# Optimization experiments

Measured on AMD Instinct MI355X. Metric: run time of the kernel, lower is better.

Reference implementation:

```python
import jax, jax.numpy as jnp
import numpy as np

B, L, D_MODEL = 8, 2048, 256
D_STATE, D_CONV, EXPAND, DT_RANK = 8, 4, 2, 2
D_INNER = EXPAND * D_MODEL
CHUNK = 32  # chunkSize in _parallelScan


def setup_inputs() -> dict:
    key = jax.random.key(0)
    ks = jax.random.split(key, 8)
    def nrm(k, shape, fan_in):
        return jax.random.normal(k, shape, jnp.float32) / np.float32(np.sqrt(fan_in))
    x = jax.random.normal(ks[0], (B, L, D_MODEL), jnp.float32)
    W_in = nrm(ks[1], (D_MODEL, 2 * D_INNER), D_MODEL)            # inProj (no bias)
    conv_w = nrm(ks[2], (D_INNER, 1, D_CONV), D_CONV)             # depthwise conv [O,I/g,K]
    conv_b = jnp.zeros((D_INNER,), jnp.float32)
    W_x = nrm(ks[3], (D_INNER, DT_RANK + 2 * D_STATE), D_INNER)   # xProj (no bias)
    dt_std = DT_RANK ** -0.5
    W_dt = jax.random.uniform(ks[4], (DT_RANK, D_INNER), jnp.float32, -dt_std, dt_std)
    u = jax.random.uniform(ks[5], (D_INNER,), jnp.float32)
    b_dt = u * np.float32(np.log(0.1) - np.log(0.001)) + np.float32(np.log(0.001))  # log(invDt)
    A_log = jnp.log(jnp.tile(jnp.arange(1, D_STATE + 1, dtype=jnp.float32), (D_INNER, 1)))
    Dp = jnp.ones((D_INNER,), jnp.float32)
    W_out = nrm(ks[6], (D_INNER, D_MODEL), D_INNER)
    pre_g = jnp.ones((D_MODEL,), jnp.float32)
    pre_b = jnp.zeros((D_MODEL,), jnp.float32)
    post_g = jnp.ones((D_MODEL,), jnp.float32)
    post_b = jnp.zeros((D_MODEL,), jnp.float32)
    return dict(x=x, pre_g=pre_g, pre_b=pre_b, post_g=post_g, post_b=post_b,
                W_in=W_in, conv_w=conv_w, conv_b=conv_b, W_x=W_x, W_dt=W_dt,
                b_dt=b_dt, A_log=A_log, Dp=Dp, W_out=W_out)


def layernorm(x, g, b, eps=1e-5):
    mu = jnp.mean(x, axis=-1, keepdims=True)
    var = jnp.var(x, axis=-1, keepdims=True)
    return (x - mu) * jax.lax.rsqrt(var + eps) * g + b


def _parallel_scan(deltaA, deltaBX, C, Dp, xc):
    # deltaA, deltaBX: [B, L, I, N]; C: [B, L, N]; xc: [B, L, I]
    Bb, Lb, I, N = deltaA.shape
    nC = Lb // CHUNK
    def chunked(t):
        return jnp.moveaxis(t.reshape((Bb, nC, CHUNK) + t.shape[2:]), 1, 0)
    cA, cBX, cC, cX = chunked(deltaA), chunked(deltaBX), chunked(C), chunked(xc)

    def body(h, inp):
        a, bx, c, xck = inp  # a,bx: [B,CHUNK,I,N]; c: [B,CHUNK,N]; xck: [B,CHUNK,I]
        logA = jnp.log(jnp.maximum(a, 1e-6))
        cum = jnp.cumsum(logA, axis=1)
        cumA = jnp.exp(jnp.minimum(cum, 20.0))
        hInit = h[:, None] * cumA
        inv = jnp.exp(-jnp.clip(cum, -20.0, 20.0))
        cumBX = jnp.cumsum(bx * inv, axis=1)
        hChunk = hInit + cumA * cumBX                      # [B,CHUNK,I,N]
        y = jnp.einsum('blin,bln->bli', hChunk, c) + xck * Dp
        return hChunk[:, -1], y

    h0 = jnp.zeros((Bb, I, N), deltaA.dtype)
    _, ys = jax.lax.scan(body, h0, (cA, cBX, cC, cX))      # ys: [nC,B,CHUNK,I]
    return jnp.moveaxis(ys, 0, 1).reshape(Bb, Lb, I)


def _ssm(x, W_in, conv_w, conv_b, W_x, W_dt, b_dt, A_log, Dp, W_out):
    Bb, Lb, _ = x.shape
    xr = x @ W_in                                          # [B,L,2I]
    xc, res = xr[..., :D_INNER], xr[..., D_INNER:]
    # depthwise causal conv (pad dConv-1 left == torch pad-both then slice [:L])
    xt = jnp.swapaxes(xc, 1, 2)                            # [B,I,L]
    xt = jax.lax.conv_general_dilated(
        xt, conv_w, window_strides=(1,), padding=[(D_CONV - 1, 0)],
        dimension_numbers=('NCH', 'OIH', 'NCH'), feature_group_count=D_INNER)
    xt = xt + conv_b[None, :, None]
    xc = jax.nn.silu(jnp.swapaxes(xt, 1, 2))               # [B,L,I]
    A = -jnp.exp(A_log.astype(jnp.float32))                # [I,N]
    xdbl = xc @ W_x
    delta = xdbl[..., :DT_RANK]
    Bm = xdbl[..., DT_RANK:DT_RANK + D_STATE]
    Cm = xdbl[..., DT_RANK + D_STATE:]
    delta = jax.nn.softplus(delta @ W_dt + b_dt)           # [B,L,I]
    deltaA = jnp.exp(delta[..., None] * A)                 # [B,L,I,N]
    deltaBX = delta[..., None] * Bm[:, :, None, :] * xc[..., None]
    y = _parallel_scan(deltaA, deltaBX, Cm, Dp.astype(jnp.float32), xc)
    y = y * jax.nn.silu(res)
    return y @ W_out


def reference(x, pre_g, pre_b, post_g, post_b, W_in, conv_w, conv_b, W_x, W_dt,
              b_dt, A_log, Dp, W_out):
    residual = x
    xn = layernorm(x, pre_g, pre_b)
    args = (W_in, conv_w, conv_b, W_x, W_dt, b_dt, A_log, Dp, W_out)
    h_fwd = _ssm(xn, *args)
    h_bwd = jnp.flip(_ssm(jnp.flip(xn, axis=1), *args), axis=1)
    out = residual + h_fwd + h_bwd                         # DropPath is identity (eval / p=0)
    return layernorm(out, post_g, post_b)
```

## Files before the change

### kernel.cpp

```cpp
#include <hip/hip_runtime.h>
#include <hip/hip_bf16.h>
#include <math.h>

#define BQ 8
#define LQ 2048
#define DM 256
#define DI 512
#define NS 8
#define NT (BQ*LQ)
#define NCH 64
#define CHK 32

typedef __attribute__((ext_vector_type(8))) __bf16 bf16x8;
typedef __attribute__((ext_vector_type(4))) float f32x4;

#define GPTR(p) ((const __attribute__((address_space(1))) void*)(p))
#define SPTR(p) ((__attribute__((address_space(3))) void*)(p))

__device__ __forceinline__ float fast_silu(float v){
  return v * __builtin_amdgcn_rcpf(1.0f + __expf(-v));
}
__device__ __forceinline__ unsigned short f2bf(float f){
  unsigned int u = __float_as_uint(f);
  unsigned int r = (u + 0x7FFFu + ((u >> 16) & 1u)) >> 16;
  return (unsigned short)r;
}
__device__ __forceinline__ float b2f(unsigned short u){
  return __uint_as_float(((unsigned int)u) << 16);
}
__device__ __forceinline__ f32x4 sp4(float x){ return (f32x4){x,x,x,x}; }

#define E20F  4.85165195e8f

__global__ __launch_bounds__(256) void prep_kernel(const float* __restrict__ W_in,
                                                   const float* __restrict__ W_out,
                                                   const float* __restrict__ W_x,
                                                   unsigned short* __restrict__ WinT,
                                                   unsigned short* __restrict__ WoutT,
                                                   unsigned short* __restrict__ WxBC,
                                                   float* __restrict__ Wdt01){
  int id = blockIdx.x*256 + threadIdx.x;
  if(id < 1024*256){ int n = id >> 8, k = id & 255; WinT[id]  = f2bf(W_in[k*1024+n]); }
  if(id < 256*512){  int n = id >> 9, k = id & 511; WoutT[id] = f2bf(W_out[k*256+n]); }
  if(id < 16*512){   int j = id >> 9, k = id & 511; WxBC[id]  = f2bf(W_x[k*18+2+j]); }
  if(id < 2*512){    int j = id >> 9, k = id & 511; Wdt01[id] = W_x[k*18+j]; }
}

template<bool OB>
__global__ __launch_bounds__(256) void ln_kernel(const float* __restrict__ in,
                                                 const float* __restrict__ g,
                                                 const float* __restrict__ bv,
                                                 void* __restrict__ outp){
  int w = threadIdx.x >> 6, lane = threadIdx.x & 63;
  size_t row = (size_t)blockIdx.x*4 + w;
  const float4* rp = (const float4*)(in + row*DM);
  float4 v = rp[lane];
  float s  = v.x+v.y+v.z+v.w;
  float sq = v.x*v.x+v.y*v.y+v.z*v.z+v.w*v.w;
  #pragma unroll
  for(int m=32;m>=1;m>>=1){ s += __shfl_xor(s,m); sq += __shfl_xor(sq,m); }
  float mean = s*(1.0f/DM);
  float var  = sq*(1.0f/DM) - mean*mean;
  float rstd = rsqrtf(var + 1e-5f);
  float4 gv = ((const float4*)g)[lane];
  float4 bb = ((const float4*)bv)[lane];
  float4 o;
  o.x = (v.x-mean)*rstd*gv.x + bb.x;
  o.y = (v.y-mean)*rstd*gv.y + bb.y;
  o.z = (v.z-mean)*rstd*gv.z + bb.z;
  o.w = (v.w-mean)*rstd*gv.w + bb.w;
  if(OB){
    ushort4 q; q.x=f2bf(o.x); q.y=f2bf(o.y); q.z=f2bf(o.z); q.w=f2bf(o.w);
    *(ushort4*)((unsigned short*)outp + row*DM + lane*4) = q;
  } else {
    ((float4*)((float*)outp + row*DM))[lane] = o;
  }
}

template<int K, bool RESID, bool OUTBF>
__global__ __launch_bounds__(256) void gemm_bf16(const unsigned short* __restrict__ A,
                                                 const unsigned short* __restrict__ Bt,
                                                 const float* __restrict__ xres,
                                                 void* __restrict__ Cv, int N){
  __shared__ unsigned short As[128*32];
  __shared__ unsigned short Bs[128*32];
  const int tid = threadIdx.x;
  const int wid = tid >> 6, lane = tid & 63;
  const int wm = wid >> 1, wn = wid & 1;
  const int row0 = blockIdx.y*128, col0 = blockIdx.x*128;
  f32x4 acc[4][4] = {};

  for(int kt = 0; kt < K; kt += 32){
    {
      int ch = tid;
      const unsigned short* ga = A + (size_t)(row0 + (ch>>2))*K + kt + (ch&3)*8;
      __builtin_amdgcn_global_load_lds(GPTR(ga), SPTR(As + wid*512), 16, 0, 0);
      const unsigned short* gb = Bt + (size_t)(col0 + (ch>>2))*K + kt + (ch&3)*8;
      __builtin_amdgcn_global_load_lds(GPTR(gb), SPTR(Bs + wid*512), 16, 0, 0);
    }
    {
      int ch = tid + 256;
      const unsigned short* ga = A + (size_t)(row0 + (ch>>2))*K + kt + (ch&3)*8;
      __builtin_amdgcn_global_load_lds(GPTR(ga), SPTR(As + 2048 + wid*512), 16, 0, 0);
      const unsigned short* gb = Bt + (size_t)(col0 + (ch>>2))*K + kt + (ch&3)*8;
      __builtin_amdgcn_global_load_lds(GPTR(gb), SPTR(Bs + 2048 + wid*512), 16, 0, 0);
    }
    __syncthreads();

    bf16x8 af[4], bfv[4];
    #pragma unroll
    for(int m=0;m<4;m++)
      af[m] = *(const bf16x8*)(const void*)&As[(wm*64 + m*16 + (lane&15))*32 + (lane>>4)*8];
    #pragma unroll
    for(int n=0;n<4;n++)
      bfv[n] = *(const bf16x8*)(const void*)&Bs[(wn*64 + n*16 + (lane&15))*32 + (lane>>4)*8];
    #pragma unroll
    for(int m=0;m<4;m++)
      #pragma unroll
      for(int n=0;n<4;n++)
        acc[m][n] = __builtin_amdgcn_mfma_f32_16x16x32_bf16(af[m], bfv[n], acc[m][n], 0, 0, 0);
    __syncthreads();
  }

  const int cr = (lane>>4)*4, cc = lane&15;
  #pragma unroll
  for(int m=0;m<4;m++){
    #pragma unroll
    for(int n=0;n<4;n++){
      int col = col0 + wn*64 + n*16 + cc;
      size_t base = (size_t)(row0 + wm*64 + m*16 + cr)*N + col;
      #pragma unroll
      for(int r=0;r<4;r++){
        float v = acc[m][n][r];
        if constexpr (OUTBF){
          ((unsigned short*)Cv)[base + (size_t)r*N] = f2bf(v);
        } else {
          if constexpr (RESID) v += xres[base + (size_t)r*N];
          ((float*)Cv)[base + (size_t)r*N] = v;
        }
      }
    }
  }
}

__global__ __launch_bounds__(256) void conv_dt_kernel(const unsigned short* __restrict__ xrb,
                                                      const float* __restrict__ cw,
                                                      const float* __restrict__ cb,
                                                      const float* __restrict__ Wdt01,
                                                      unsigned short* __restrict__ xbf_f,
                                                      unsigned short* __restrict__ xbf_b,
                                                      float* __restrict__ dt2f,
                                                      float* __restrict__ dt2b){
  const int tid = threadIdx.x;
  const int tok = tid >> 7, q = tid & 127;
  const int i = q*4;
  const size_t row = (size_t)blockIdx.x*2 + tok;
  const int l = (int)(row & (LQ-1));

  float4 wc0 = *(const float4*)&cw[(i+0)*4];
  float4 wc1 = *(const float4*)&cw[(i+1)*4];
  float4 wc2 = *(const float4*)&cw[(i+2)*4];
  float4 wc3 = *(const float4*)&cw[(i+3)*4];
  float4 bias = *(const float4*)&cb[i];

  float4 r[7];
  #pragma unroll
  for(int d=0; d<7; d++){
    int off = d-3;
    bool ok = (l+off >= 0) && (l+off < LQ);
    if(ok){
      ushort4 t4 = *(const ushort4*)&xrb[(row+off)*1024 + i];
      r[d] = make_float4(b2f(t4.x), b2f(t4.y), b2f(t4.z), b2f(t4.w));
    } else r[d] = make_float4(0.f,0.f,0.f,0.f);
  }
  float4 sf = bias;
  sf.x += r[0].x*wc0.x + r[1].x*wc0.y + r[2].x*wc0.z + r[3].x*wc0.w;
  sf.y += r[0].y*wc1.x + r[1].y*wc1.y + r[2].y*wc1.z + r[3].y*wc1.w;
  sf.z += r[0].z*wc2.x + r[1].z*wc2.y + r[2].z*wc2.z + r[3].z*wc2.w;
  sf.w += r[0].w*wc3.x + r[1].w*wc3.y + r[2].w*wc3.z + r[3].w*wc3.w;
  float4 sb = bias;
  sb.x += r[6].x*wc0.x + r[5].x*wc0.y + r[4].x*wc0.z + r[3].x*wc0.w;
  sb.y += r[6].y*wc1.x + r[5].y*wc1.y + r[4].y*wc1.z + r[3].y*wc1.w;
  sb.z += r[6].z*wc2.x + r[5].z*wc2.y + r[4].z*wc2.z + r[3].z*wc2.w;
  sb.w += r[6].w*wc3.x + r[5].w*wc3.y + r[4].w*wc3.z + r[3].w*wc3.w;

  float4 of, ob;
  of.x = fast_silu(sf.x); of.y = fast_silu(sf.y); of.z = fast_silu(sf.z); of.w = fast_silu(sf.w);
  ob.x = fast_silu(sb.x); ob.y = fast_silu(sb.y); ob.z = fast_silu(sb.z); ob.w = fast_silu(sb.w);

  size_t e = row*512 + i;
  ushort4 obf; obf.x=f2bf(of.x); obf.y=f2bf(of.y); obf.z=f2bf(of.z); obf.w=f2bf(of.w);
  *(ushort4*)&xbf_f[e] = obf;
  ushort4 obb; obb.x=f2bf(ob.x); obb.y=f2bf(ob.y); obb.z=f2bf(ob.z); obb.w=f2bf(ob.w);
  *(ushort4*)&xbf_b[e] = obb;

  float4 w0q = *(const float4*)&Wdt01[i];
  float4 w1q = *(const float4*)&Wdt01[512+i];
  float s0f = of.x*w0q.x + of.y*w0q.y + of.z*w0q.z + of.w*w0q.w;
  float s1f = of.x*w1q.x + of.y*w1q.y + of.z*w1q.z + of.w*w1q.w;
  float s0b = ob.x*w0q.x + ob.y*w0q.y + ob.z*w0q.z + ob.w*w0q.w;
  float s1b = ob.x*w1q.x + ob.y*w1q.y + ob.z*w1q.z + ob.w*w1q.w;
  #pragma unroll
  for(int m=32;m>=1;m>>=1){
    s0f += __shfl_xor(s0f,m); s1f += __shfl_xor(s1f,m);
    s0b += __shfl_xor(s0b,m); s1b += __shfl_xor(s1b,m);
  }
  __shared__ float red[4][4];
  int wid = tid >> 6;
  if((tid & 63) == 0){ red[wid][0]=s0f; red[wid][1]=s1f; red[wid][2]=s0b; red[wid][3]=s1b; }
  __syncthreads();
  if(tid == 0){
    size_t r0 = (size_t)blockIdx.x*2;
    dt2f[r0*2+0] = red[0][0]+red[1][0];  dt2f[r0*2+1] = red[0][1]+red[1][1];
    dt2b[r0*2+0] = red[0][2]+red[1][2];  dt2b[r0*2+1] = red[0][3]+red[1][3];
  }
  if(tid == 128){
    size_t r1 = (size_t)blockIdx.x*2 + 1;
    dt2f[r1*2+0] = red[2][0]+red[3][0];  dt2f[r1*2+1] = red[2][1]+red[3][1];
    dt2b[r1*2+0] = red[2][2]+red[3][2];  dt2b[r1*2+1] = red[2][3]+red[3][3];
  }
}

__global__ __launch_bounds__(256) void bc_gemm(const unsigned short* __restrict__ xbf_f,
                                               const unsigned short* __restrict__ xbf_b,
                                               const unsigned short* __restrict__ WxBC,
                                               float* __restrict__ BCf,
                                               float* __restrict__ BCb){
  int dir = blockIdx.y;
  const unsigned short* A = dir ? xbf_b : xbf_f;
  float* BC = dir ? BCb : BCf;
  const int row0 = blockIdx.x*256;
  __shared__ unsigned short As[256*32];
  __shared__ unsigned short Bs[16*32];
  const int tid = threadIdx.x, wid = tid>>6, lane = tid&63;
  f32x4 acc[4] = {};
  for(int kt=0; kt<512; kt+=32){
    #pragma unroll
    for(int r=0;r<4;r++){
      int ch = r*256 + tid;
      const unsigned short* ga = A + (size_t)(row0 + (ch>>2))*512 + kt + (ch&3)*8;
      __builtin_amdgcn_global_load_lds(GPTR(ga), SPTR(As + r*2048 + wid*512), 16, 0, 0);
    }
    if(wid==0){
      int ch = lane;
      const unsigned short* gb = WxBC + (size_t)(ch>>2)*512 + kt + (ch&3)*8;
      __builtin_amdgcn_global_load_lds(GPTR(gb), SPTR(Bs), 16, 0, 0);
    }
    __syncthreads();
    bf16x8 bfv = *(const bf16x8*)(const void*)&Bs[(lane&15)*32 + (lane>>4)*8];
    #pragma unroll
    for(int m=0;m<4;m++){
      bf16x8 af = *(const bf16x8*)(const void*)&As[(wid*64 + m*16 + (lane&15))*32 + (lane>>4)*8];
      acc[m] = __builtin_amdgcn_mfma_f32_16x16x32_bf16(af, bfv, acc[m], 0, 0, 0);
    }
    __syncthreads();
  }
  const int cr = (lane>>4)*4, cc = lane&15;
  #pragma unroll
  for(int m=0;m<4;m++)
    #pragma unroll
    for(int r=0;r<4;r++)
      BC[(size_t)(row0 + wid*64 + m*16 + cr + r)*16 + cc] = acc[m][r];
}


__global__ __launch_bounds__(256) void scan_pass1(
    const float* __restrict__ dt2f, const float* __restrict__ dt2b,
    const float* __restrict__ BCf,  const float* __restrict__ BCb,
    const unsigned short* __restrict__ xbf_f, const unsigned short* __restrict__ xbf_b,
    const float* __restrict__ Wdt,  const float* __restrict__ bdt,
    float* __restrict__ a_arr, float* __restrict__ b_arr){
  int dir = blockIdx.z, b = blockIdx.y;
  int chunk = blockIdx.x >> 1, ib = blockIdx.x & 1;
  int i = ib*256 + threadIdx.x;
  const float* dt2 = dir ? dt2b : dt2f;
  const float* BC  = dir ? BCb  : BCf;
  const unsigned short* xc = dir ? xbf_b : xbf_f;
  float w0 = Wdt[i], w1 = Wdt[512+i], bd = bdt[i];
  f32x4 cAA = sp4(1.f), cAB = sp4(1.f), SA = sp4(0.f), SB = sp4(0.f);
  #pragma unroll 2
  for(int t=0;t<CHK;t++){
    int p = chunk*CHK + t;
    int l = dir ? (LQ-1-p) : p;
    size_t row = (size_t)b*LQ + l;
    float d0 = dt2[row*2+0], d1 = dt2[row*2+1];
    float dpre = d0*w0 + d1*w1 + bd;
    float t0 = __expf(fminf(dpre, 80.f));
    float ep = 1.f + t0;
    float e1 = __builtin_amdgcn_rcpf(ep);
    float delta = __logf(ep);
    float dxv = delta * b2f(xc[row*512+i]);
    const f32x4* bc4 = (const f32x4*)&BC[row*16];
    f32x4 bmA = bc4[0], bmB = bc4[1];
    float e2=e1*e1, e4=e2*e2;
    f32x4 pdA = {e1, e2, e2*e1, e4};
    f32x4 pdB = pdA * e4;
    f32x4 emA = __builtin_elementwise_max(pdA, sp4(1e-6f));
    f32x4 emB = __builtin_elementwise_max(pdB, sp4(1e-6f));
    cAA *= emA;  cAB *= emB;
    f32x4 wA = __builtin_elementwise_min(cAA*E20F, sp4(1.f));
    f32x4 wB = __builtin_elementwise_min(cAB*E20F, sp4(1.f));
    SA = emA*SA + (bmA*wA)*dxv;
    SB = emB*SB + (bmB*wB)*dxv;
  }
  size_t base = (size_t)((dir*BQ + b)*NCH + chunk)*4096 + i;
  #pragma unroll
  for(int n=0;n<4;n++){
    a_arr[base + n*512]     = cAA[n];
    a_arr[base + (n+4)*512] = cAB[n];
    b_arr[base + n*512]     = SA[n];
    b_arr[base + (n+4)*512] = SB[n];
  }
}

__global__ __launch_bounds__(256) void scan_pass2(float* __restrict__ a_arr,
                                                  const float* __restrict__ b_arr){
  int dir = blockIdx.z, b = blockIdx.y;
  int j = blockIdx.x*256 + threadIdx.x;
  size_t base = (size_t)(dir*BQ + b)*NCH*4096 + j;
  float h = 0.f;
  for(int c=0;c<NCH;c++){
    size_t idx = base + (size_t)c*4096;
    float a = a_arr[idx], bb = b_arr[idx];
    a_arr[idx] = h;
    h = a*h + bb;
  }
}

__global__ __launch_bounds__(128) void scan_pass3z(
    const float* __restrict__ dt2f, const float* __restrict__ dt2b,
    const float* __restrict__ BCf,  const float* __restrict__ BCb,
    const unsigned short* __restrict__ xbf_f, const unsigned short* __restrict__ xbf_b,
    const unsigned short* __restrict__ xrb,
    const float* __restrict__ Wdt,  const float* __restrict__ bdt,
    const float* __restrict__ Dpv,  const float* __restrict__ hin,
    unsigned short* __restrict__ z){
  __shared__ float yfs[CHK][128];
  int b = blockIdx.y;
  int c = blockIdx.x >> 2, ic = blockIdx.x & 3;
  int tid = threadIdx.x;
  int i = ic*128 + tid;
  float w0 = Wdt[i], w1 = Wdt[512+i], bd = bdt[i], dp = Dpv[i];

  {
    size_t base = (size_t)(((size_t)b)*NCH + c)*4096 + i;
    f32x4 h0A = {hin[base+0*512], hin[base+1*512], hin[base+2*512], hin[base+3*512]};
    f32x4 h0B = {hin[base+4*512], hin[base+5*512], hin[base+6*512], hin[base+7*512]};
    f32x4 cAA = sp4(1.f), cAB = sp4(1.f), SA = sp4(0.f), SB = sp4(0.f);
    #pragma unroll 2
    for(int t=0;t<CHK;t++){
      size_t row = (size_t)b*LQ + c*CHK + t;
      float d0 = dt2f[row*2+0], d1 = dt2f[row*2+1];
      float dpre = d0*w0 + d1*w1 + bd;
      float t0 = __expf(fminf(dpre, 80.f));
      float ep = 1.f + t0;
      float e1 = __builtin_amdgcn_rcpf(ep);
      float delta = __logf(ep);
      float xv = b2f(xbf_f[row*512+i]);
      float dxv = delta*xv;
      const f32x4* bc4 = (const f32x4*)&BCf[row*16];
      f32x4 bmA = bc4[0], bmB = bc4[1], cmA = bc4[2], cmB = bc4[3];
      float e2=e1*e1, e4=e2*e2;
      f32x4 pdA = {e1, e2, e2*e1, e4};
      f32x4 pdB = pdA * e4;
      f32x4 emA = __builtin_elementwise_max(pdA, sp4(1e-6f));
      f32x4 emB = __builtin_elementwise_max(pdB, sp4(1e-6f));
      cAA *= emA;  cAB *= emB;
      f32x4 wA = __builtin_elementwise_min(cAA*E20F, sp4(1.f));
      f32x4 wB = __builtin_elementwise_min(cAB*E20F, sp4(1.f));
      SA = emA*SA + (bmA*wA)*dxv;
      SB = emB*SB + (bmB*wB)*dxv;
      f32x4 yv = (cAA*h0A + SA)*cmA + (cAB*h0B + SB)*cmB;
      yfs[t][tid] = xv*dp + yv[0] + yv[1] + yv[2] + yv[3];
    }
  }
  {
    int cb_ = NCH-1-c;
    size_t base = (size_t)(((size_t)BQ + b)*NCH + cb_)*4096 + i;
    f32x4 h0A = {hin[base+0*512], hin[base+1*512], hin[base+2*512], hin[base+3*512]};
    f32x4 h0B = {hin[base+4*512], hin[base+5*512], hin[base+6*512], hin[base+7*512]};
    f32x4 cAA = sp4(1.f), cAB = sp4(1.f), SA = sp4(0.f), SB = sp4(0.f);
    #pragma unroll 2
    for(int t=0;t<CHK;t++){
      int l = c*CHK + (CHK-1-t);
      size_t row = (size_t)b*LQ + l;
      float d0 = dt2b[row*2+0], d1 = dt2b[row*2+1];
      float dpre = d0*w0 + d1*w1 + bd;
      float t0 = __expf(fminf(dpre, 80.f));
      float ep = 1.f + t0;
      float e1 = __builtin_amdgcn_rcpf(ep);
      float delta = __logf(ep);
      float xv = b2f(xbf_b[row*512+i]);
      float dxv = delta*xv;
      const f32x4* bc4 = (const f32x4*)&BCb[row*16];
      f32x4 bmA = bc4[0], bmB = bc4[1], cmA = bc4[2], cmB = bc4[3];
      float e2=e1*e1, e4=e2*e2;
      f32x4 pdA = {e1, e2, e2*e1, e4};
      f32x4 pdB = pdA * e4;
      f32x4 emA = __builtin_elementwise_max(pdA, sp4(1e-6f));
      f32x4 emB = __builtin_elementwise_max(pdB, sp4(1e-6f));
      cAA *= emA;  cAB *= emB;
      f32x4 wA = __builtin_elementwise_min(cAA*E20F, sp4(1.f));
      f32x4 wB = __builtin_elementwise_min(cAB*E20F, sp4(1.f));
      SA = emA*SA + (bmA*wA)*dxv;
      SB = emB*SB + (bmB*wB)*dxv;
      f32x4 yv = (cAA*h0A + SA)*cmA + (cAB*h0B + SB)*cmB;
      float yb = xv*dp + yv[0] + yv[1] + yv[2] + yv[3];
      float yf = yfs[CHK-1-t][tid];
      float res = b2f(xrb[row*1024 + 512 + i]);
      z[row*512 + i] = f2bf((yf + yb) * fast_silu(res));
    }
  }
}

extern "C" void kernel_launch(void* const* d_in, const int* in_sizes, int n_in,
                              void* d_out, int out_size, void* d_ws, size_t ws_size,
                              hipStream_t stream) {
  const float* x      = (const float*)d_in[0];
  const float* pre_g  = (const float*)d_in[1];
  const float* pre_b  = (const float*)d_in[2];
  const float* post_g = (const float*)d_in[3];
  const float* post_b = (const float*)d_in[4];
  const float* W_in   = (const float*)d_in[5];
  const float* conv_w = (const float*)d_in[6];
  const float* conv_b = (const float*)d_in[7];
  const float* W_x    = (const float*)d_in[8];
  const float* W_dt   = (const float*)d_in[9];
  const float* b_dt   = (const float*)d_in[10];
  const float* Dp     = (const float*)d_in[12];
  const float* W_out  = (const float*)d_in[13];
  float* out = (float*)d_out;

  float* ws    = (float*)d_ws;
  float* xr32  = ws;
  unsigned short* xr_bf = (unsigned short*)xr32;
  float* xn32  = xr32  + (size_t)NT*1024;
  float* xcfr  = xn32  + (size_t)NT*256;
  unsigned short* xbf_f = (unsigned short*)xcfr;
  float* xcbr  = xcfr  + (size_t)NT*512;
  unsigned short* xbf_b = (unsigned short*)xcbr;
  float* dt2f  = xcbr  + (size_t)NT*512;
  float* dt2b  = dt2f  + (size_t)NT*2;
  float* BCf   = dt2b  + (size_t)NT*2;
  float* BCb   = BCf   + (size_t)NT*16;
  float* a_arr = BCb   + (size_t)NT*16;
  float* b_arr = a_arr + (size_t)2*BQ*NCH*NS*DI;
  unsigned short* WinT  = (unsigned short*)(b_arr + (size_t)2*BQ*NCH*NS*DI);
  unsigned short* WoutT = WinT + 1024*256;
  unsigned short* WxBC  = WoutT + 256*512;
  float* Wdt01          = (float*)(WxBC + 16*512);
  unsigned short* xn_bf = (unsigned short*)a_arr;
  unsigned short* z_bf  = (unsigned short*)b_arr;

  prep_kernel<<<1024, 256, 0, stream>>>(W_in, W_out, W_x, WinT, WoutT, WxBC, Wdt01);
  ln_kernel<true><<<NT/4, 256, 0, stream>>>(x, pre_g, pre_b, xn_bf);
  gemm_bf16<256,false,true><<<dim3(1024/128, NT/128), 256, 0, stream>>>(xn_bf, WinT, nullptr, xr_bf, 1024);
  conv_dt_kernel<<<NT/2, 256, 0, stream>>>(xr_bf, conv_w, conv_b, Wdt01,
                                           xbf_f, xbf_b, dt2f, dt2b);
  bc_gemm<<<dim3(NT/256, 2), 256, 0, stream>>>(xbf_f, xbf_b, WxBC, BCf, BCb);
  scan_pass1<<<dim3(NCH*2, BQ, 2), 256, 0, stream>>>(dt2f, dt2b, BCf, BCb, xbf_f, xbf_b,
                                                     W_dt, b_dt, a_arr, b_arr);
  scan_pass2<<<dim3(16, BQ, 2), 256, 0, stream>>>(a_arr, b_arr);
  scan_pass3z<<<dim3(NCH*4, BQ), 128, 0, stream>>>(dt2f, dt2b, BCf, BCb, xbf_f, xbf_b, xr_bf,
                                                   W_dt, b_dt, Dp, a_arr, z_bf);
  gemm_bf16<512,true,false><<<dim3(256/128, NT/128), 256, 0, stream>>>(z_bf, WoutT, x, xn32, 256);
  ln_kernel<false><<<NT/4, 256, 0, stream>>>(xn32, post_g, post_b, out);
}
```

Baseline: 187.4 us.

## Fuse output projection with residual add and post-LayerNorm; simplify scan recurrences

Replaces the output GEMM plus separate post-LayerNorm kernel with one kernel. It computes full 256-column rows per block (64 rows, 512 threads), adds the residual, and reduces row statistics through shuffles and LDS. This removes the fp32 intermediate write and read and one launch, but gives a grid of only 256 blocks. The scan passes also drop the separate cumulative-A and S accumulators in favour of a scaled running product and a direct state recurrence with the initial state folded in, which cuts per-step multiplies.

```diff
diff --git a/kernel.cpp b/kernel.cpp
--- a/kernel.cpp
+++ b/kernel.cpp
@@ -30,7 +30,8 @@
 }
 __device__ __forceinline__ f32x4 sp4(float x){ return (f32x4){x,x,x,x}; }
 
-#define E20F  4.85165195e8f
+#define E20F   4.85165195e8f
+#define EM20F  2.06115369e-9f
 
 __global__ __launch_bounds__(256) void prep_kernel(const float* __restrict__ W_in,
                                                    const float* __restrict__ W_out,
@@ -46,11 +47,10 @@
   if(id < 2*512){    int j = id >> 9, k = id & 511; Wdt01[id] = W_x[k*18+j]; }
 }
 
-template<bool OB>
 __global__ __launch_bounds__(256) void ln_kernel(const float* __restrict__ in,
                                                  const float* __restrict__ g,
                                                  const float* __restrict__ bv,
-                                                 void* __restrict__ outp){
+                                                 unsigned short* __restrict__ outp){
   int w = threadIdx.x >> 6, lane = threadIdx.x & 63;
   size_t row = (size_t)blockIdx.x*4 + w;
   const float4* rp = (const float4*)(in + row*DM);
@@ -64,24 +64,18 @@
   float rstd = rsqrtf(var + 1e-5f);
   float4 gv = ((const float4*)g)[lane];
   float4 bb = ((const float4*)bv)[lane];
-  float4 o;
-  o.x = (v.x-mean)*rstd*gv.x + bb.x;
-  o.y = (v.y-mean)*rstd*gv.y + bb.y;
-  o.z = (v.z-mean)*rstd*gv.z + bb.z;
-  o.w = (v.w-mean)*rstd*gv.w + bb.w;
-  if(OB){
-    ushort4 q; q.x=f2bf(o.x); q.y=f2bf(o.y); q.z=f2bf(o.z); q.w=f2bf(o.w);
-    *(ushort4*)((unsigned short*)outp + row*DM + lane*4) = q;
-  } else {
-    ((float4*)((float*)outp + row*DM))[lane] = o;
-  }
-}
-
-template<int K, bool RESID, bool OUTBF>
+  ushort4 q;
+  q.x = f2bf((v.x-mean)*rstd*gv.x + bb.x);
+  q.y = f2bf((v.y-mean)*rstd*gv.y + bb.y);
+  q.z = f2bf((v.z-mean)*rstd*gv.z + bb.z);
+  q.w = f2bf((v.w-mean)*rstd*gv.w + bb.w);
+  *(ushort4*)(outp + row*DM + lane*4) = q;
+}
+
+template<int K>
 __global__ __launch_bounds__(256) void gemm_bf16(const unsigned short* __restrict__ A,
                                                  const unsigned short* __restrict__ Bt,
-                                                 const float* __restrict__ xres,
-                                                 void* __restrict__ Cv, int N){
+                                                 unsigned short* __restrict__ C, int N){
   __shared__ unsigned short As[128*32];
   __shared__ unsigned short Bs[128*32];
   const int tid = threadIdx.x;
@@ -124,23 +118,110 @@
 
   const int cr = (lane>>4)*4, cc = lane&15;
   #pragma unroll
-  for(int m=0;m<4;m++){
+  for(int m=0;m<4;m++)
     #pragma unroll
     for(int n=0;n<4;n++){
       int col = col0 + wn*64 + n*16 + cc;
       size_t base = (size_t)(row0 + wm*64 + m*16 + cr)*N + col;
       #pragma unroll
-      for(int r=0;r<4;r++){
-        float v = acc[m][n][r];
-        if constexpr (OUTBF){
-          ((unsigned short*)Cv)[base + (size_t)r*N] = f2bf(v);
-        } else {
-          if constexpr (RESID) v += xres[base + (size_t)r*N];
-          ((float*)Cv)[base + (size_t)r*N] = v;
-        }
+      for(int r=0;r<4;r++)
+        C[base + (size_t)r*N] = f2bf(acc[m][n][r]);
+    }
+}
+
+__global__ __launch_bounds__(512) void gemm_out_ln(const unsigned short* __restrict__ A,
+                                                   const unsigned short* __restrict__ Bt,
+                                                   const float* __restrict__ xres,
+                                                   const float* __restrict__ g,
+                                                   const float* __restrict__ bv,
+                                                   float* __restrict__ out){
+  __shared__ unsigned short As[64*32];
+  __shared__ unsigned short Bs[256*32];
+  __shared__ float red_s[64][4];
+  __shared__ float red_q[64][4];
+  __shared__ float ln_m[64];
+  __shared__ float ln_r[64];
+  const int tid = threadIdx.x;
+  const int wid = tid >> 6, lane = tid & 63;
+  const int wm = wid >> 2, wn = wid & 3;
+  const int row0 = blockIdx.x*64;
+  f32x4 acc[2][4] = {};
+
+  for(int kt = 0; kt < 512; kt += 32){
+    if(wid < 4){
+      int ch = wid*64 + lane;
+      const unsigned short* ga = A + (size_t)(row0 + (ch>>2))*512 + kt + (ch&3)*8;
+      __builtin_amdgcn_global_load_lds(GPTR(ga), SPTR(As + wid*512), 16, 0, 0);
+    }
+    #pragma unroll
+    for(int r=0;r<2;r++){
+      int ch = r*512 + tid;
+      const unsigned short* gb = Bt + (size_t)(ch>>2)*512 + kt + (ch&3)*8;
+      __builtin_amdgcn_global_load_lds(GPTR(gb), SPTR(Bs + r*4096 + wid*512), 16, 0, 0);
+    }
+    __syncthreads();
+
+    bf16x8 af[2], bfv[4];
+    #pragma unroll
+    for(int m=0;m<2;m++)
+      af[m] = *(const bf16x8*)(const void*)&As[(wm*32 + m*16 + (lane&15))*32 + (lane>>4)*8];
+    #pragma unroll
+    for(int n=0;n<4;n++)
+      bfv[n] = *(const bf16x8*)(const void*)&Bs[(wn*64 + n*16 + (lane&15))*32 + (lane>>4)*8];
+    #pragma unroll
+    for(int m=0;m<2;m++)
+      #pragma unroll
+      for(int n=0;n<4;n++)
+        acc[m][n] = __builtin_amdgcn_mfma_f32_16x16x32_bf16(af[m], bfv[n], acc[m][n], 0, 0, 0);
+    __syncthreads();
+  }
+
+  const int cr = (lane>>4)*4, cc = lane&15;
+  #pragma unroll
+  for(int m=0;m<2;m++){
+    #pragma unroll
+    for(int r=0;r<4;r++){
+      int row = wm*32 + m*16 + cr + r;
+      float s = 0.f, qq = 0.f;
+      #pragma unroll
+      for(int n=0;n<4;n++){
+        int col = wn*64 + n*16 + cc;
+        float v = acc[m][n][r] + xres[(size_t)(row0+row)*256 + col];
+        acc[m][n][r] = v;
+        s += v; qq += v*v;
       }
-    }
-  }
+      s += __shfl_xor(s,1); qq += __shfl_xor(qq,1);
+      s += __shfl_xor(s,2); qq += __shfl_xor(qq,2);
+      s += __shfl_xor(s,4); qq += __shfl_xor(qq,4);
+      s += __shfl_xor(s,8); qq += __shfl_xor(qq,8);
+      if((lane&15)==0){ red_s[row][wn] = s; red_q[row][wn] = qq; }
+    }
+  }
+  __syncthreads();
+  if(tid < 64){
+    float S = red_s[tid][0]+red_s[tid][1]+red_s[tid][2]+red_s[tid][3];
+    float Q = red_q[tid][0]+red_q[tid][1]+red_q[tid][2]+red_q[tid][3];
+    float mean = S*(1.f/256.f);
+    float var  = Q*(1.f/256.f) - mean*mean;
+    ln_m[tid] = mean;
+    ln_r[tid] = rsqrtf(var + 1e-5f);
+  }
+  __syncthreads();
+  float gq[4], bq[4];
+  #pragma unroll
+  for(int n=0;n<4;n++){ int col = wn*64+n*16+cc; gq[n] = g[col]; bq[n] = bv[col]; }
+  #pragma unroll
+  for(int m=0;m<2;m++)
+    #pragma unroll
+    for(int r=0;r<4;r++){
+      int row = wm*32 + m*16 + cr + r;
+      float mean = ln_m[row], rstd = ln_r[row];
+      #pragma unroll
+      for(int n=0;n<4;n++){
+        int col = wn*64 + n*16 + cc;
+        out[(size_t)(row0+row)*256 + col] = (acc[m][n][r]-mean)*rstd*gq[n] + bq[n];
+      }
+    }
 }
 
 __global__ __launch_bounds__(256) void conv_dt_kernel(const unsigned short* __restrict__ xrb,
@@ -277,7 +358,7 @@
   const float* BC  = dir ? BCb  : BCf;
   const unsigned short* xc = dir ? xbf_b : xbf_f;
   float w0 = Wdt[i], w1 = Wdt[512+i], bd = bdt[i];
-  f32x4 cAA = sp4(1.f), cAB = sp4(1.f), SA = sp4(0.f), SB = sp4(0.f);
+  f32x4 qA = sp4(E20F), qB = sp4(E20F), hA = sp4(0.f), hB = sp4(0.f);
   #pragma unroll 2
   for(int t=0;t<CHK;t++){
     int p = chunk*CHK + t;
@@ -297,19 +378,20 @@
     f32x4 pdB = pdA * e4;
     f32x4 emA = __builtin_elementwise_max(pdA, sp4(1e-6f));
     f32x4 emB = __builtin_elementwise_max(pdB, sp4(1e-6f));
-    cAA *= emA;  cAB *= emB;
-    f32x4 wA = __builtin_elementwise_min(cAA*E20F, sp4(1.f));
-    f32x4 wB = __builtin_elementwise_min(cAB*E20F, sp4(1.f));
-    SA = emA*SA + (bmA*wA)*dxv;
-    SB = emB*SB + (bmB*wB)*dxv;
+    qA *= emA;  qB *= emB;
+    f32x4 wA = __builtin_elementwise_min(qA, sp4(1.f));
+    f32x4 wB = __builtin_elementwise_min(qB, sp4(1.f));
+    hA = emA*hA + (bmA*wA)*dxv;
+    hB = emB*hB + (bmB*wB)*dxv;
   }
   size_t base = (size_t)((dir*BQ + b)*NCH + chunk)*4096 + i;
+  f32x4 aA = qA*EM20F, aB = qB*EM20F;
   #pragma unroll
   for(int n=0;n<4;n++){
-    a_arr[base + n*512]     = cAA[n];
-    a_arr[base + (n+4)*512] = cAB[n];
-    b_arr[base + n*512]     = SA[n];
-    b_arr[base + (n+4)*512] = SB[n];
+    a_arr[base + n*512]     = aA[n];
+    a_arr[base + (n+4)*512] = aB[n];
+    b_arr[base + n*512]     = hA[n];
+    b_arr[base + (n+4)*512] = hB[n];
   }
 }
 
@@ -344,9 +426,9 @@
 
   {
     size_t base = (size_t)(((size_t)b)*NCH + c)*4096 + i;
-    f32x4 h0A = {hin[base+0*512], hin[base+1*512], hin[base+2*512], hin[base+3*512]};
-    f32x4 h0B = {hin[base+4*512], hin[base+5*512], hin[base+6*512], hin[base+7*512]};
-    f32x4 cAA = sp4(1.f), cAB = sp4(1.f), SA = sp4(0.f), SB = sp4(0.f);
+    f32x4 hA = {hin[base+0*512], hin[base+1*512], hin[base+2*512], hin[base+3*512]};
+    f32x4 hB = {hin[base+4*512], hin[base+5*512], hin[base+6*512], hin[base+7*512]};
+    f32x4 qA = sp4(E20F), qB = sp4(E20F);
     #pragma unroll 2
     for(int t=0;t<CHK;t++){
       size_t row = (size_t)b*LQ + c*CHK + t;
@@ -365,21 +447,21 @@
       f32x4 pdB = pdA * e4;
       f32x4 emA = __builtin_elementwise_max(pdA, sp4(1e-6f));
       f32x4 emB = __builtin_elementwise_max(pdB, sp4(1e-6f));
-      cAA *= emA;  cAB *= emB;
-      f32x4 wA = __builtin_elementwise_min(cAA*E20F, sp4(1.f));
-      f32x4 wB = __builtin_elementwise_min(cAB*E20F, sp4(1.f));
-      SA = emA*SA + (bmA*wA)*dxv;
-      SB = emB*SB + (bmB*wB)*dxv;
-      f32x4 yv = (cAA*h0A + SA)*cmA + (cAB*h0B + SB)*cmB;
+      qA *= emA;  qB *= emB;
+      f32x4 wA = __builtin_elementwise_min(qA, sp4(1.f));
+      f32x4 wB = __builtin_elementwise_min(qB, sp4(1.f));
+      hA = emA*hA + (bmA*wA)*dxv;
+      hB = emB*hB + (bmB*wB)*dxv;
+      f32x4 yv = hA*cmA + hB*cmB;
       yfs[t][tid] = xv*dp + yv[0] + yv[1] + yv[2] + yv[3];
     }
   }
   {
     int cb_ = NCH-1-c;
     size_t base = (size_t)(((size_t)BQ + b)*NCH + cb_)*4096 + i;
-    f32x4 h0A = {hin[base+0*512], hin[base+1*512], hin[base+2*512], hin[base+3*512]};
-    f32x4 h0B = {hin[base+4*512], hin[base+5*512], hin[base+6*512], hin[base+7*512]};
-    f32x4 cAA = sp4(1.f), cAB = sp4(1.f), SA = sp4(0.f), SB = sp4(0.f);
+    f32x4 hA = {hin[base+0*512], hin[base+1*512], hin[base+2*512], hin[base+3*512]};
+    f32x4 hB = {hin[base+4*512], hin[base+5*512], hin[base+6*512], hin[base+7*512]};
+    f32x4 qA = sp4(E20F), qB = sp4(E20F);
     #pragma unroll 2
     for(int t=0;t<CHK;t++){
       int l = c*CHK + (CHK-1-t);
@@ -399,12 +481,12 @@
       f32x4 pdB = pdA * e4;
       f32x4 emA = __builtin_elementwise_max(pdA, sp4(1e-6f));
       f32x4 emB = __builtin_elementwise_max(pdB, sp4(1e-6f));
-      cAA *= emA;  cAB *= emB;
-      f32x4 wA = __builtin_elementwise_min(cAA*E20F, sp4(1.f));
-      f32x4 wB = __builtin_elementwise_min(cAB*E20F, sp4(1.f));
-      SA = emA*SA + (bmA*wA)*dxv;
-      SB = emB*SB + (bmB*wB)*dxv;
-      f32x4 yv = (cAA*h0A + SA)*cmA + (cAB*h0B + SB)*cmB;
+      qA *= emA;  qB *= emB;
+      f32x4 wA = __builtin_elementwise_min(qA, sp4(1.f));
+      f32x4 wB = __builtin_elementwise_min(qB, sp4(1.f));
+      hA = emA*hA + (bmA*wA)*dxv;
+      hB = emB*hB + (bmB*wB)*dxv;
+      f32x4 yv = hA*cmA + hB*cmB;
       float yb = xv*dp + yv[0] + yv[1] + yv[2] + yv[3];
       float yf = yfs[CHK-1-t][tid];
       float res = b2f(xrb[row*1024 + 512 + i]);
@@ -453,8 +535,8 @@
   unsigned short* z_bf  = (unsigned short*)b_arr;
 
   prep_kernel<<<1024, 256, 0, stream>>>(W_in, W_out, W_x, WinT, WoutT, WxBC, Wdt01);
-  ln_kernel<true><<<NT/4, 256, 0, stream>>>(x, pre_g, pre_b, xn_bf);
-  gemm_bf16<256,false,true><<<dim3(1024/128, NT/128), 256, 0, stream>>>(xn_bf, WinT, nullptr, xr_bf, 1024);
+  ln_kernel<<<NT/4, 256, 0, stream>>>(x, pre_g, pre_b, xn_bf);
+  gemm_bf16<256><<<dim3(1024/128, NT/128), 256, 0, stream>>>(xn_bf, WinT, xr_bf, 1024);
   conv_dt_kernel<<<NT/2, 256, 0, stream>>>(xr_bf, conv_w, conv_b, Wdt01,
                                            xbf_f, xbf_b, dt2f, dt2b);
   bc_gemm<<<dim3(NT/256, 2), 256, 0, stream>>>(xbf_f, xbf_b, WxBC, BCf, BCb);
@@ -463,6 +545,5 @@
   scan_pass2<<<dim3(16, BQ, 2), 256, 0, stream>>>(a_arr, b_arr);
   scan_pass3z<<<dim3(NCH*4, BQ), 128, 0, stream>>>(dt2f, dt2b, BCf, BCb, xbf_f, xbf_b, xr_bf,
                                                    W_dt, b_dt, Dp, a_arr, z_bf);
-  gemm_bf16<512,true,false><<<dim3(256/128, NT/128), 256, 0, stream>>>(z_bf, WoutT, x, xn32, 256);
-  ln_kernel<false><<<NT/4, 256, 0, stream>>>(xn32, post_g, post_b, out);
-}
+  gemm_out_ln<<<NT/64, 512, 0, stream>>>(z_bf, WoutT, x, post_g, post_b, out);
+}
```

New measurement: 180.9 us. -3.5%, faster.
